# Performance work log

Measured on AMD Instinct MI355X. Metric: run time of the kernel, lower is better.

Reference implementation:

```python
import jax, jax.numpy as jnp
import numpy as np

DIM = 1024
HEADS = 16
HEAD_DIM = DIM // HEADS


def setup_inputs() -> dict:
    key = jax.random.key(0)
    ks = jax.random.split(key, 9)
    x = jax.random.normal(ks[0], (2, 2048, DIM), dtype=jnp.float32)
    s = 1.0 / np.sqrt(DIM)
    Wq = jax.random.normal(ks[1], (DIM, DIM), dtype=jnp.float32) * s
    bq = jax.random.normal(ks[2], (DIM,), dtype=jnp.float32) * s
    Wk = jax.random.normal(ks[3], (DIM, DIM), dtype=jnp.float32) * s
    bk = jax.random.normal(ks[4], (DIM,), dtype=jnp.float32) * s
    Wv = jax.random.normal(ks[5], (DIM, DIM), dtype=jnp.float32) * s
    bv = jax.random.normal(ks[6], (DIM,), dtype=jnp.float32) * s
    Wo = jax.random.normal(ks[7], (DIM, DIM), dtype=jnp.float32) * s
    bo = jax.random.normal(ks[8], (DIM,), dtype=jnp.float32) * s
    return {"x": x, "Wq": Wq, "bq": bq, "Wk": Wk, "bk": bk,
            "Wv": Wv, "bv": bv, "Wo": Wo, "bo": bo}


def reference(x, Wq, bq, Wk, bk, Wv, bv, Wo, bo):
    B, S, _ = x.shape
    # projections (torch Linear: x @ W.T + b; here W stored as [in, out])
    q = x @ Wq + bq
    k = x @ Wk + bk  # context = x (self-attention)
    v = x @ Wv + bv
    # [B, H, S, Dh]
    q = q.reshape(B, S, HEADS, HEAD_DIM).transpose(0, 2, 1, 3)
    k = k.reshape(B, S, HEADS, HEAD_DIM).transpose(0, 2, 1, 3)
    v = v.reshape(B, S, HEADS, HEAD_DIM).transpose(0, 2, 1, 3)
    scores = jnp.einsum('bhqd,bhkd->bhqk', q, k) / np.sqrt(HEAD_DIM).astype(np.float32)
    weights = jax.nn.softmax(scores, axis=-1)
    emb = jnp.einsum('bhqk,bhkd->bhqd', weights, v)
    emb = emb.transpose(0, 2, 1, 3).reshape(B, S, DIM)
    return emb @ Wo + bo
```

## Files before the change

kernel.cpp:

```cpp
#include <hip/hip_runtime.h>
#include <hip/hip_bf16.h>
#include <stdint.h>

typedef __attribute__((ext_vector_type(8))) short short8;
typedef __attribute__((ext_vector_type(4))) float f32x4;
typedef __attribute__((ext_vector_type(4))) unsigned int uint4v;

#define DIMW 1024
#define HEADS 16
#define HEAD_DIM 64
#define SEQ 2048
#define BATCH 2
#define MTOK 4096
#define QKVN 3072
#define QKN 2048
#define QSCALE 0.1803368801111204f

typedef const __attribute__((address_space(1))) unsigned int* gas_u32p;
typedef __attribute__((address_space(3))) unsigned int* las_u32p;

static __device__ __forceinline__ void gl_lds16(const void* g, void* l) {
    __builtin_amdgcn_global_load_lds((gas_u32p)g, (las_u32p)l, 16, 0, 0);
}

static __device__ __forceinline__ unsigned short f2bf(float f) {
    unsigned int u = __float_as_uint(f);
    u += 0x7fffu + ((u >> 16) & 1u);
    return (unsigned short)(u >> 16);
}

__global__ void cast_x_kernel(const float* __restrict__ x, unsigned short* __restrict__ out) {
    int i = (blockIdx.x * 256 + threadIdx.x) * 8;
    float4 a = *(const float4*)(x + i);
    float4 b = *(const float4*)(x + i + 4);
    unsigned short t[8] = { f2bf(a.x), f2bf(a.y), f2bf(a.z), f2bf(a.w),
                            f2bf(b.x), f2bf(b.y), f2bf(b.z), f2bf(b.w) };
    *(uint4v*)(out + i) = *(const uint4v*)t;
}

__global__ void prep_w_kernel(const float* __restrict__ Wq, const float* __restrict__ Wk,
                              const float* __restrict__ Wv, const float* __restrict__ Wo,
                              unsigned short* __restrict__ Wqkv_t, unsigned short* __restrict__ Wo_t) {
    __shared__ float tile[64][68];
    int z = blockIdx.z;
    const float* W = (z == 0) ? Wq : (z == 1) ? Wk : (z == 2) ? Wv : Wo;
    unsigned short* out = (z < 3) ? (Wqkv_t + (size_t)z * DIMW * DIMW) : Wo_t;
    int n0 = blockIdx.x * 64, k0 = blockIdx.y * 64;
    int tid = threadIdx.x;
    for (int it = 0; it < 4; ++it) {
        int c = it * 256 + tid;
        int r = c >> 4, cg = c & 15;
        float4 v = *(const float4*)(W + (size_t)(k0 + r) * DIMW + n0 + cg * 4);
        tile[r][cg * 4 + 0] = v.x; tile[r][cg * 4 + 1] = v.y;
        tile[r][cg * 4 + 2] = v.z; tile[r][cg * 4 + 3] = v.w;
    }
    __syncthreads();
    for (int it = 0; it < 2; ++it) {
        int c = it * 256 + tid;
        int n = c >> 3, kg = c & 7;
        unsigned short tmp[8];
        #pragma unroll
        for (int j = 0; j < 8; ++j) tmp[j] = f2bf(tile[kg * 8 + j][n]);
        *(uint4v*)(out + (size_t)(n0 + n) * DIMW + k0 + kg * 8) = *(const uint4v*)tmp;
    }
}

template<int MI, bool QKV3, typename TO>
__global__ __launch_bounds__(256, 3) void gemm_bt_kernel(
    const unsigned short* __restrict__ A, const unsigned short* __restrict__ Bt,
    const float* __restrict__ b0, const float* __restrict__ b1, const float* __restrict__ b2,
    TO* __restrict__ C, unsigned short* __restrict__ Vt, int M, int N, int K, int ldc)
{
    __shared__ __align__(16) unsigned short As[MI * 32 * 32];
    __shared__ __align__(16) unsigned short Bs[128 * 32];
    int tid = threadIdx.x;
    int wave = tid >> 6, lane = tid & 63;
    int lrow = lane & 15, quad = lane >> 4;
    int bm = blockIdx.y * (MI * 32), bn = blockIdx.x * 128;
    int wm = (wave >> 1) * (MI * 16), wn = (wave & 1) * 64;
    int sw = (lrow >> 1) & 3;
    f32x4 acc[MI][4];
    #pragma unroll
    for (int i = 0; i < MI; ++i)
        #pragma unroll
        for (int j = 0; j < 4; ++j) acc[i][j] = (f32x4){0.f, 0.f, 0.f, 0.f};
    const unsigned short* Ap = A + (size_t)bm * K;
    const unsigned short* Bp = Bt + (size_t)bn * K;
    for (int k0 = 0; k0 < K; k0 += 32) {
        __syncthreads();
        #pragma unroll
        for (int it = 0; it < MI / 2; ++it) {
            int c = it * 256 + tid;
            int ch = (c & 3) ^ ((c >> 3) & 3);
            gl_lds16(Ap + (size_t)(c >> 2) * K + k0 + ch * 8, &As[c * 8]);
        }
        #pragma unroll
        for (int it = 0; it < 2; ++it) {
            int c = it * 256 + tid;
            int ch = (c & 3) ^ ((c >> 3) & 3);
            gl_lds16(Bp + (size_t)(c >> 2) * K + k0 + ch * 8, &Bs[c * 8]);
        }
        __syncthreads();
        short8 af[MI], bfr[4];
        #pragma unroll
        for (int mi = 0; mi < MI; ++mi)
            af[mi] = *(const short8*)&As[(wm + mi * 16 + lrow) * 32 + (quad ^ sw) * 8];
        #pragma unroll
        for (int ni = 0; ni < 4; ++ni)
            bfr[ni] = *(const short8*)&Bs[(wn + ni * 16 + lrow) * 32 + (quad ^ sw) * 8];
        #pragma unroll
        for (int mi = 0; mi < MI; ++mi)
            #pragma unroll
            for (int ni = 0; ni < 4; ++ni)
                acc[mi][ni] = __builtin_amdgcn_mfma_f32_16x16x32_bf16(af[mi], bfr[ni], acc[mi][ni], 0, 0, 0);
    }
    #pragma unroll
    for (int ni = 0; ni < 4; ++ni) {
        int n = bn + wn + ni * 16 + lrow;
        float bias, scale;
        int sel = 0;
        if (QKV3) {
            sel = n >> 10;
            const float* bp = (sel == 0) ? b0 : (sel == 1) ? b1 : b2;
            bias = bp[n & 1023];
            scale = (sel == 0) ? QSCALE : 1.0f;
        } else { bias = b0[n]; scale = 1.0f; }
        #pragma unroll
        for (int mi = 0; mi < MI; ++mi) {
            int m0 = bm + wm + mi * 16 + quad * 4;
            if (QKV3 && sel == 2) {
                int vcol = n - 2048;
                int bb = m0 >> 11, s0 = m0 & 2047;
                unsigned short t[4];
                #pragma unroll
                for (int i = 0; i < 4; ++i) t[i] = f2bf(acc[mi][ni][i] + bias);
                *(uint2*)(Vt + ((size_t)(bb * 1024 + vcol)) * SEQ + s0) = *(const uint2*)t;
            } else {
                #pragma unroll
                for (int i = 0; i < 4; ++i) {
                    float val = (acc[mi][ni][i] + bias) * scale;
                    if constexpr (sizeof(TO) == 2) C[(size_t)(m0 + i) * ldc + n] = (TO)f2bf(val);
                    else                           C[(size_t)(m0 + i) * ldc + n] = val;
                }
            }
        }
    }
}

__global__ __launch_bounds__(256, 3) void attn_kernel(
    const unsigned short* __restrict__ Qk, const unsigned short* __restrict__ Vt,
    unsigned short* __restrict__ Op, float* __restrict__ L)
{
    __shared__ __align__(16) unsigned short Ks[128 * 64];
    __shared__ __align__(16) unsigned short Vs[64 * 128];
    __shared__ __align__(16) unsigned short Ps[4][32 * 32];
    int tid = threadIdx.x;
    int wave = tid >> 6, lane = tid & 63;
    int lrow = lane & 15, quad = lane >> 4;
    int h = blockIdx.x, qblk = blockIdx.y;
    int b = blockIdx.z >> 1, split = blockIdx.z & 1;
    int q0 = qblk * 128 + wave * 32;
    const unsigned short* Qbase = Qk + (size_t)(b * SEQ) * QKN + h * 64;
    const unsigned short* Kbase = Qk + (size_t)(b * SEQ) * QKN + 1024 + h * 64;
    const unsigned short* Vtb = Vt + (size_t)(b * 1024 + h * 64) * SEQ;

    short8 qf[2][2];
    #pragma unroll
    for (int mi = 0; mi < 2; ++mi)
        #pragma unroll
        for (int kc = 0; kc < 2; ++kc)
            qf[mi][kc] = *(const short8*)(Qbase + (size_t)(q0 + mi * 16 + lrow) * QKN + kc * 32 + quad * 8);

    f32x4 o[2][4];
    float lrun[2] = {0.f, 0.f};
    #pragma unroll
    for (int mi = 0; mi < 2; ++mi)
        #pragma unroll
        for (int ont = 0; ont < 4; ++ont) o[mi][ont] = (f32x4){0.f, 0.f, 0.f, 0.f};

    int kchunk = ((lane & 7) ^ (lane >> 3)) * 8;
    int swk = lrow & 7;
    int psw = (lrow & 6) << 2;

    int kv_lo = split * 1024;
    for (int kv0 = kv_lo; kv0 < kv_lo + 1024; kv0 += 128) {
        __syncthreads();
        #pragma unroll
        for (int it = 0; it < 4; ++it) {
            int r0 = wave * 32 + it * 8;
            gl_lds16(Kbase + (size_t)(kv0 + r0 + (lane >> 3)) * QKN + kchunk,
                     &Ks[r0 * 64 + lane * 8]);
        }
        #pragma unroll
        for (int it = 0; it < 4; ++it) {
            int d0 = wave * 16 + it * 4;
            int vc = ((lane & 15) ^ ((it * 4 + (lane >> 4)) & 15)) * 8;
            gl_lds16(Vtb + (size_t)(d0 + (lane >> 4)) * SEQ + kv0 + vc,
                     &Vs[d0 * 128 + lane * 8]);
        }
        __syncthreads();

        int p01[2][8], p23[2][8];
        #pragma unroll
        for (int half = 0; half < 2; ++half) {
            f32x4 s[2][4];
            #pragma unroll
            for (int mi = 0; mi < 2; ++mi)
                #pragma unroll
                for (int nt2 = 0; nt2 < 4; ++nt2) s[mi][nt2] = (f32x4){0.f, 0.f, 0.f, 0.f};
            #pragma unroll
            for (int nt2 = 0; nt2 < 4; ++nt2) {
                int r = (half * 4 + nt2) * 16 + lrow;
                short8 kf0 = *(const short8*)&Ks[r * 64 + (quad ^ swk) * 8];
                short8 kf1 = *(const short8*)&Ks[r * 64 + ((4 + quad) ^ swk) * 8];
                #pragma unroll
                for (int mi = 0; mi < 2; ++mi) {
                    s[mi][nt2] = __builtin_amdgcn_mfma_f32_16x16x32_bf16(kf0, qf[mi][0], s[mi][nt2], 0, 0, 0);
                    s[mi][nt2] = __builtin_amdgcn_mfma_f32_16x16x32_bf16(kf1, qf[mi][1], s[mi][nt2], 0, 0, 0);
                }
            }
            #pragma unroll
            for (int mi = 0; mi < 2; ++mi)
                #pragma unroll
                for (int nt2 = 0; nt2 < 4; ++nt2) {
                    f32x4 p;
                    #pragma unroll
                    for (int c2 = 0; c2 < 4; ++c2) {
                        p[c2] = __builtin_amdgcn_exp2f(s[mi][nt2][c2]);
                        lrun[mi] += p[c2];
                    }
                    __hip_bfloat162 a01 = __float22bfloat162_rn(float2{p[0], p[1]});
                    __hip_bfloat162 a23 = __float22bfloat162_rn(float2{p[2], p[3]});
                    p01[mi][half * 4 + nt2] = *reinterpret_cast<int*>(&a01);
                    p23[mi][half * 4 + nt2] = *reinterpret_cast<int*>(&a23);
                }
        }

        #pragma unroll
        for (int kc = 0; kc < 4; ++kc) {
            #pragma unroll
            for (int mi = 0; mi < 2; ++mi)
                #pragma unroll
                for (int h2 = 0; h2 < 2; ++h2) {
                    int nt = kc * 2 + h2;
                    uint2 pk;
                    pk.x = (unsigned int)p01[mi][nt];
                    pk.y = (unsigned int)p23[mi][nt];
                    *(uint2*)&Ps[wave][(mi * 16 + lrow) * 32 + (((h2 * 4 + quad) << 2) ^ psw)] = pk;
                }
            short8 af0 = *(const short8*)&Ps[wave][lrow * 32 + (((quad * 2) << 2) ^ psw)];
            short8 af1 = *(const short8*)&Ps[wave][(16 + lrow) * 32 + (((quad * 2) << 2) ^ psw)];
            #pragma unroll
            for (int ont = 0; ont < 4; ++ont) {
                int rv = ont * 16 + lrow;
                int pos = ((kc * 4 + quad) ^ lrow) * 8;
                short8 vf = *(const short8*)&Vs[rv * 128 + pos];
                o[0][ont] = __builtin_amdgcn_mfma_f32_16x16x32_bf16(af0, vf, o[0][ont], 0, 0, 0);
                o[1][ont] = __builtin_amdgcn_mfma_f32_16x16x32_bf16(af1, vf, o[1][ont], 0, 0, 0);
            }
        }
    }

    #pragma unroll
    for (int mi = 0; mi < 2; ++mi) {
        float l = lrun[mi];
        l += __shfl_xor(l, 16);
        l += __shfl_xor(l, 32);
        #pragma unroll
        for (int ont = 0; ont < 4; ++ont)
            #pragma unroll
            for (int c2 = 0; c2 < 4; ++c2) {
                size_t row = (size_t)((split * 2 + b) * SEQ + q0 + mi * 16 + quad * 4 + c2);
                Op[row * DIMW + h * 64 + ont * 16 + lrow] = f2bf(o[mi][ont][c2]);
            }
        if (quad == 0)
            L[(((size_t)(split * 2 + b) * 16 + h) * SEQ) + q0 + mi * 16 + lrow] = l;
    }
}

__global__ void combine_kernel(const unsigned short* __restrict__ Op,
                               const float* __restrict__ L,
                               unsigned short* __restrict__ Emb)
{
    int e = (blockIdx.x * 256 + threadIdx.x) * 4;
    int row = e >> 10, c = e & 1023, h = c >> 6;
    int b = row >> 11, q = row & 2047;
    float l1 = L[((size_t)(0 + b) * 16 + h) * SEQ + q];
    float l2 = L[((size_t)(2 + b) * 16 + h) * SEQ + q];
    float inv = 1.0f / (l1 + l2);
    uint2 o1 = *(const uint2*)(Op + e);
    uint2 o2 = *(const uint2*)(Op + 4194304 + e);
    unsigned short t[4];
    unsigned int parts1[4] = { o1.x << 16, o1.x & 0xffff0000u, o1.y << 16, o1.y & 0xffff0000u };
    unsigned int parts2[4] = { o2.x << 16, o2.x & 0xffff0000u, o2.y << 16, o2.y & 0xffff0000u };
    #pragma unroll
    for (int j = 0; j < 4; ++j) {
        float f1 = __uint_as_float(parts1[j]);
        float f2 = __uint_as_float(parts2[j]);
        t[j] = f2bf((f1 + f2) * inv);
    }
    *(uint2*)(Emb + e) = *(const uint2*)t;
}

extern "C" void kernel_launch(void* const* d_in, const int* in_sizes, int n_in,
                              void* d_out, int out_size, void* d_ws, size_t ws_size,
                              hipStream_t stream)
{
    const float* x  = (const float*)d_in[0];
    const float* Wq = (const float*)d_in[1];
    const float* bq = (const float*)d_in[2];
    const float* Wk = (const float*)d_in[3];
    const float* bk = (const float*)d_in[4];
    const float* Wv = (const float*)d_in[5];
    const float* bv = (const float*)d_in[6];
    const float* Wo = (const float*)d_in[7];
    const float* bo = (const float*)d_in[8];
    float* out = (float*)d_out;
    char* ws = (char*)d_ws;

    unsigned short* Xbf   = (unsigned short*)(ws);
    unsigned short* Wqkvt = (unsigned short*)(ws + 8388608);
    unsigned short* Wot   = (unsigned short*)(ws + 14680064);
    unsigned short* Qk    = (unsigned short*)(ws + 16777216);
    unsigned short* Vt    = (unsigned short*)(ws + 33554432);
    unsigned short* Emb   = (unsigned short*)(ws + 41943040);
    unsigned short* Op    = (unsigned short*)(ws + 50331648);
    float*          L     = (float*)(ws + 67108864);

    cast_x_kernel<<<2048, 256, 0, stream>>>(x, Xbf);
    prep_w_kernel<<<dim3(16, 16, 4), 256, 0, stream>>>(Wq, Wk, Wv, Wo, Wqkvt, Wot);
    gemm_bt_kernel<4, true, unsigned short><<<dim3(24, 32), 256, 0, stream>>>(
        Xbf, Wqkvt, bq, bk, bv, Qk, Vt, MTOK, QKVN, DIMW, QKN);
    attn_kernel<<<dim3(16, 16, 4), 256, 0, stream>>>(Qk, Vt, Op, L);
    combine_kernel<<<4096, 256, 0, stream>>>(Op, L, Emb);
    gemm_bt_kernel<2, false, float><<<dim3(8, 64), 256, 0, stream>>>(
        Emb, Wot, bo, nullptr, nullptr, out, nullptr, MTOK, DIMW, DIMW, DIMW);
}
```

Before: 211.5 us.

## Double GEMM K-step to 64 and stage V-transpose epilogue through LDS

The projection GEMM now loads a 64-wide K slab per iteration, with a new 8-way XOR swizzle, and issues two MFMA sub-steps per slab. This halves the number of barrier pairs and global-to-LDS round trips per tile. The V-slice epilogue now writes biased bf16 values into a padded LDS tile and then stores full 16-byte coalesced rows into Vt, replacing the scattered 8-byte transposed stores. LDS use per block grows, which may reduce occupancy under the 3-blocks launch bound.

```diff
diff --git a/kernel.cpp b/kernel.cpp
--- a/kernel.cpp
+++ b/kernel.cpp
@@ -71,14 +71,19 @@
     const float* __restrict__ b0, const float* __restrict__ b1, const float* __restrict__ b2,
     TO* __restrict__ C, unsigned short* __restrict__ Vt, int M, int N, int K, int ldc)
 {
-    __shared__ __align__(16) unsigned short As[MI * 32 * 32];
-    __shared__ __align__(16) unsigned short Bs[128 * 32];
+    constexpr int STAGE = MI * 32 * 64 + 128 * 64;
+    constexpr int TSZ = QKV3 ? 128 * 136 : 0;
+    constexpr int SMEMN = STAGE > TSZ ? STAGE : TSZ;
+    __shared__ __align__(16) unsigned short Smem[SMEMN];
+    unsigned short* As = Smem;
+    unsigned short* Bs = Smem + MI * 32 * 64;
+
     int tid = threadIdx.x;
     int wave = tid >> 6, lane = tid & 63;
     int lrow = lane & 15, quad = lane >> 4;
     int bm = blockIdx.y * (MI * 32), bn = blockIdx.x * 128;
     int wm = (wave >> 1) * (MI * 16), wn = (wave & 1) * 64;
-    int sw = (lrow >> 1) & 3;
+    int sw = lrow & 7;
     f32x4 acc[MI][4];
     #pragma unroll
     for (int i = 0; i < MI; ++i)
@@ -86,56 +91,74 @@
         for (int j = 0; j < 4; ++j) acc[i][j] = (f32x4){0.f, 0.f, 0.f, 0.f};
     const unsigned short* Ap = A + (size_t)bm * K;
     const unsigned short* Bp = Bt + (size_t)bn * K;
-    for (int k0 = 0; k0 < K; k0 += 32) {
-        __syncthreads();
-        #pragma unroll
-        for (int it = 0; it < MI / 2; ++it) {
+    for (int k0 = 0; k0 < K; k0 += 64) {
+        __syncthreads();
+        #pragma unroll
+        for (int it = 0; it < MI; ++it) {
             int c = it * 256 + tid;
-            int ch = (c & 3) ^ ((c >> 3) & 3);
-            gl_lds16(Ap + (size_t)(c >> 2) * K + k0 + ch * 8, &As[c * 8]);
-        }
-        #pragma unroll
-        for (int it = 0; it < 2; ++it) {
+            int row = c >> 3, pos = c & 7;
+            gl_lds16(Ap + (size_t)row * K + k0 + (pos ^ (row & 7)) * 8, &As[c * 8]);
+        }
+        #pragma unroll
+        for (int it = 0; it < 4; ++it) {
             int c = it * 256 + tid;
-            int ch = (c & 3) ^ ((c >> 3) & 3);
-            gl_lds16(Bp + (size_t)(c >> 2) * K + k0 + ch * 8, &Bs[c * 8]);
-        }
-        __syncthreads();
-        short8 af[MI], bfr[4];
-        #pragma unroll
-        for (int mi = 0; mi < MI; ++mi)
-            af[mi] = *(const short8*)&As[(wm + mi * 16 + lrow) * 32 + (quad ^ sw) * 8];
-        #pragma unroll
-        for (int ni = 0; ni < 4; ++ni)
-            bfr[ni] = *(const short8*)&Bs[(wn + ni * 16 + lrow) * 32 + (quad ^ sw) * 8];
-        #pragma unroll
-        for (int mi = 0; mi < MI; ++mi)
+            int row = c >> 3, pos = c & 7;
+            gl_lds16(Bp + (size_t)row * K + k0 + (pos ^ (row & 7)) * 8, &Bs[c * 8]);
+        }
+        __syncthreads();
+        #pragma unroll
+        for (int t = 0; t < 2; ++t) {
+            short8 af[MI], bfr[4];
+            #pragma unroll
+            for (int mi = 0; mi < MI; ++mi)
+                af[mi] = *(const short8*)&As[(wm + mi * 16 + lrow) * 64 + ((t * 4 + quad) ^ sw) * 8];
             #pragma unroll
             for (int ni = 0; ni < 4; ++ni)
-                acc[mi][ni] = __builtin_amdgcn_mfma_f32_16x16x32_bf16(af[mi], bfr[ni], acc[mi][ni], 0, 0, 0);
-    }
-    #pragma unroll
-    for (int ni = 0; ni < 4; ++ni) {
-        int n = bn + wn + ni * 16 + lrow;
-        float bias, scale;
-        int sel = 0;
-        if (QKV3) {
-            sel = n >> 10;
-            const float* bp = (sel == 0) ? b0 : (sel == 1) ? b1 : b2;
-            bias = bp[n & 1023];
-            scale = (sel == 0) ? QSCALE : 1.0f;
-        } else { bias = b0[n]; scale = 1.0f; }
-        #pragma unroll
-        for (int mi = 0; mi < MI; ++mi) {
-            int m0 = bm + wm + mi * 16 + quad * 4;
-            if (QKV3 && sel == 2) {
-                int vcol = n - 2048;
-                int bb = m0 >> 11, s0 = m0 & 2047;
-                unsigned short t[4];
-                #pragma unroll
-                for (int i = 0; i < 4; ++i) t[i] = f2bf(acc[mi][ni][i] + bias);
-                *(uint2*)(Vt + ((size_t)(bb * 1024 + vcol)) * SEQ + s0) = *(const uint2*)t;
-            } else {
+                bfr[ni] = *(const short8*)&Bs[(wn + ni * 16 + lrow) * 64 + ((t * 4 + quad) ^ sw) * 8];
+            #pragma unroll
+            for (int mi = 0; mi < MI; ++mi)
+                #pragma unroll
+                for (int ni = 0; ni < 4; ++ni)
+                    acc[mi][ni] = __builtin_amdgcn_mfma_f32_16x16x32_bf16(af[mi], bfr[ni], acc[mi][ni], 0, 0, 0);
+        }
+    }
+
+    int sel = QKV3 ? (bn >> 10) : 0;
+    if (QKV3 && sel == 2) {
+        __syncthreads();
+        unsigned short* T = Smem;
+        #pragma unroll
+        for (int ni = 0; ni < 4; ++ni) {
+            int v = wn + ni * 16 + lrow;
+            float bias = b2[(bn & 1023) + v];
+            #pragma unroll
+            for (int mi = 0; mi < MI; ++mi) {
+                int s0 = wm + mi * 16 + quad * 4;
+                unsigned short t4[4];
+                #pragma unroll
+                for (int i = 0; i < 4; ++i) t4[i] = f2bf(acc[mi][ni][i] + bias);
+                *(uint2*)&T[v * 136 + s0] = *(const uint2*)t4;
+            }
+        }
+        __syncthreads();
+        int bb = bm >> 11, s_base = bm & 2047;
+        #pragma unroll
+        for (int it = 0; it < MI * 2; ++it) {
+            int c = it * 256 + tid;
+            int v = c >> (MI == 4 ? 4 : 3), ch = c & (MI == 4 ? 15 : 7);
+            uint4v val = *(const uint4v*)&T[v * 136 + ch * 8];
+            *(uint4v*)(Vt + ((size_t)(bb * 1024 + (bn - 2048) + v)) * SEQ + s_base + ch * 8) = val;
+        }
+    } else {
+        const float* bp = QKV3 ? ((sel == 0) ? b0 : b1) : b0;
+        float scale = (QKV3 && sel == 0) ? QSCALE : 1.0f;
+        #pragma unroll
+        for (int ni = 0; ni < 4; ++ni) {
+            int n = bn + wn + ni * 16 + lrow;
+            float bias = bp[QKV3 ? (n & 1023) : n];
+            #pragma unroll
+            for (int mi = 0; mi < MI; ++mi) {
+                int m0 = bm + wm + mi * 16 + quad * 4;
                 #pragma unroll
                 for (int i = 0; i < 4; ++i) {
                     float val = (acc[mi][ni][i] + bias) * scale;
```

Result: no change. 215.1 us (+1.7%).
